# Optimization experiments

Measured on AMD Instinct MI355X. Metric: run time of the kernel, lower is better.

The kernel has to match this reference:

```python
import jax, jax.numpy as jnp
import numpy as np

B, Q, S, D, H, F = 16, 8, 4096, 2048, 16, 128  # batch, new tokens, past kv, d_state, heads, head_dim
W_SCALE = 0.02  # keep projections well-conditioned for stable softmax


def setup_inputs() -> dict:
    key = jax.random.key(0)
    ks = jax.random.split(key, 8)
    return {
        "x": jax.random.normal(ks[0], (B, Q, D), jnp.float32),
        "cache_k": jax.random.normal(ks[1], (B, S, H, F), jnp.float32),
        "cache_v": jax.random.normal(ks[2], (B, S, H, F), jnp.float32),
        "wq": jax.random.normal(ks[3], (D, H, F), jnp.float32) * W_SCALE,
        "bq": jnp.zeros((H, F), jnp.float32),
        "wk": jax.random.normal(ks[4], (D, H, F), jnp.float32) * W_SCALE,
        "bk": jnp.zeros((H, F), jnp.float32),
        "wv": jax.random.normal(ks[5], (D, H, F), jnp.float32) * W_SCALE,
        "bv": jnp.zeros((H, F), jnp.float32),
        "wo": jax.random.normal(ks[6], (H, F, D), jnp.float32) * W_SCALE,
        "bo": jnp.zeros((D,), jnp.float32),
    }


def reference(x, cache_k, cache_v, wq, bq, wk, bk, wv, bv, wo, bo):
    # QKV projections: DenseGeneral(features=(H, F), axis=-1)
    q = jnp.einsum("bqd,dhf->bqhf", x, wq) + bq          # [B,Q,H,F]
    k_new = jnp.einsum("bqd,dhf->bqhf", x, wk) + bk      # [B,Q,H,F]
    v_new = jnp.einsum("bqd,dhf->bqhf", x, wv) + bv
    # concat-based KV cache growth along the sequence axis (axis=1)
    k = jnp.concatenate([cache_k, k_new], axis=1)        # [B,S+Q,H,F]
    v = jnp.concatenate([cache_v, v_new], axis=1)
    # full dot-product attention over the whole cache (mask=None on decode path)
    scale = 1.0 / jnp.sqrt(jnp.asarray(F, q.dtype))
    scores = jnp.einsum("bqhf,bkhf->bhqk", q, k) * scale  # [B,H,Q,S+Q]
    probs = jax.nn.softmax(scores, axis=-1)
    attn = jnp.einsum("bhqk,bkhf->bhqf", probs, v)        # [B,H,Q,F]
    # output projection: DenseGeneral(features=D, axis=(-3,-1)) contracts (H, F)
    out = jnp.einsum("bhqf,hfd->bqd", attn, wo) + bo      # [B,Q,D]
    return (out, k, v)
```

## Files before the change

kernel.cpp:

```cpp
#include <hip/hip_runtime.h>
#include <hip/hip_bf16.h>

constexpr int Bc = 16;
constexpr int Qc = 8;
constexpr int Sc = 4096;
constexpr int Dc = 2048;
constexpr int Hc = 16;
constexpr int Fc = 128;
constexpr int SP = Sc + Qc;
constexpr int Mr = Bc * Qc;
constexpr int CHUNK = 512;
constexpr int NCHUNK = 9;
constexpr float SCALE = 0.08838834764831845f;
constexpr float LOG2E = 1.4426950408889634f;
constexpr float QSCALE = SCALE * LOG2E;
constexpr int GKS = 8;
constexpr int GKC = Dc / GKS;

typedef float floatx4 __attribute__((ext_vector_type(4)));

__device__ __forceinline__ float4 nt_load4(const float* p) {
    floatx4 r = __builtin_nontemporal_load(reinterpret_cast<const floatx4*>(p));
    return make_float4(r.x, r.y, r.z, r.w);
}
__device__ __forceinline__ void nt_store4(float* p, float4 v) {
    floatx4 r; r.x = v.x; r.y = v.y; r.z = v.z; r.w = v.w;
    __builtin_nontemporal_store(r, reinterpret_cast<floatx4*>(p));
}

__global__ __launch_bounds__(256)
void gemm_ksplit(const float* __restrict__ A, const float* __restrict__ W0,
                 const float* __restrict__ W1, const float* __restrict__ W2,
                 float* __restrict__ part)
{
    const int ntile = blockIdx.x;
    const int mat   = blockIdx.y;
    const int kz    = blockIdx.z;
    const float* __restrict__ W = (mat == 0) ? W0 : ((mat == 1) ? W1 : W2);
    const int t  = threadIdx.x;
    const int tx = t & 15, ty = t >> 4;
    const int r0 = ty * 8, c0 = tx * 8;
    const int ncol0 = ntile * 128;

    __shared__ float a_s[128][17];
    __shared__ float w_s[16][128];

    float acc[8][8] = {};

    const int kbase = kz * GKC;
    for (int k0 = kbase; k0 < kbase + GKC; k0 += 16) {
        {
            const int kk = t & 15, r = t >> 4;
            #pragma unroll
            for (int i = 0; i < 8; i++)
                a_s[r + i * 16][kk] = A[(size_t)(r + i * 16) * Dc + k0 + kk];
        }
        {
            const int nn = t & 127, ks_ = t >> 7;
            #pragma unroll
            for (int i = 0; i < 8; i++)
                w_s[ks_ + i * 2][nn] = W[(size_t)(k0 + ks_ + i * 2) * 2048 + ncol0 + nn];
        }
        __syncthreads();
        #pragma unroll
        for (int kk = 0; kk < 16; kk++) {
            float av[8], wv[8];
            #pragma unroll
            for (int i = 0; i < 8; i++) av[i] = a_s[r0 + i][kk];
            #pragma unroll
            for (int j = 0; j < 8; j++) wv[j] = w_s[kk][c0 + j];
            #pragma unroll
            for (int i = 0; i < 8; i++)
                #pragma unroll
                for (int j = 0; j < 8; j++)
                    acc[i][j] += av[i] * wv[j];
        }
        __syncthreads();
    }
    float* __restrict__ dst = part + (size_t)(mat * GKS + kz) * Mr * 2048;
    #pragma unroll
    for (int i = 0; i < 8; i++)
        #pragma unroll
        for (int j = 0; j < 8; j++)
            dst[(size_t)(r0 + i) * 2048 + ncol0 + c0 + j] = acc[i][j];
}

__global__ __launch_bounds__(256)
void reduce_qkv(const float* __restrict__ part, const float* __restrict__ bq,
                const float* __restrict__ bk, const float* __restrict__ bv,
                float* __restrict__ q_ws, float* __restrict__ out_k, float* __restrict__ out_v)
{
    const int mat = blockIdx.y;
    const int e4 = blockIdx.x * 256 + threadIdx.x;
    const int e = e4 * 4;
    const int m = e >> 11, n = e & 2047;
    const float* __restrict__ p = part + (size_t)mat * GKS * (Mr * 2048);
    float4 s = make_float4(0, 0, 0, 0);
    #pragma unroll
    for (int ks = 0; ks < GKS; ks++) {
        const float4 a = *reinterpret_cast<const float4*>(&p[(size_t)ks * (Mr * 2048) + e]);
        s.x += a.x; s.y += a.y; s.z += a.z; s.w += a.w;
    }
    const int b = m >> 3, qi = m & 7;
    if (mat == 0) {
        const float4 bb = *reinterpret_cast<const float4*>(&bq[n]);
        s.x += bb.x; s.y += bb.y; s.z += bb.z; s.w += bb.w;
        *reinterpret_cast<float4*>(&q_ws[e]) = s;
    } else if (mat == 1) {
        const float4 bb = *reinterpret_cast<const float4*>(&bk[n]);
        s.x += bb.x; s.y += bb.y; s.z += bb.z; s.w += bb.w;
        *reinterpret_cast<float4*>(&out_k[((size_t)(b * SP + Sc + qi)) * 2048 + n]) = s;
    } else {
        const float4 bb = *reinterpret_cast<const float4*>(&bv[n]);
        s.x += bb.x; s.y += bb.y; s.z += bb.z; s.w += bb.w;
        *reinterpret_cast<float4*>(&out_v[((size_t)(b * SP + Sc + qi)) * 2048 + n]) = s;
    }
}

template<bool TAIL, int LEN>
__global__ __launch_bounds__(256, 3)
void attn_fused(const float* __restrict__ cache_k, const float* __restrict__ cache_v,
                const float* __restrict__ q_ws,
                float* __restrict__ out_k, float* __restrict__ out_v,
                float* __restrict__ part_acc, float* __restrict__ part_l)
{
    const int c = TAIL ? 8 : blockIdx.x;
    const int h = blockIdx.y;
    const int b = blockIdx.z;
    const int t = threadIdx.x;
    const int w = t >> 6;
    const int lane = t & 63;
    const int half = lane >> 5;
    const int fl = lane & 31;
    const int s0 = c * CHUNK;

    constexpr int kpw = LEN / 4;
    constexpr int pairs = LEN / 8;

    __shared__ float wacc[4][Qc][Fc];
    __shared__ float l_w[4][Qc];

    const int sel1 = fl & 1, sel2 = (fl >> 1) & 1, sel3 = (fl >> 2) & 1;
    const int myqi = 4 * sel1 + 2 * sel2 + sel3;
    int baddr[Qc];
    #pragma unroll
    for (int qi = 0; qi < Qc; qi++) {
        const int slot = ((qi >> 2) & 1) | (((qi >> 1) & 1) << 1) | ((qi & 1) << 2);
        baddr[qi] = (lane & ~7) | slot;
    }

    float4 qreg[Qc];
    #pragma unroll
    for (int qi = 0; qi < Qc; qi++) {
        float4 qv = *reinterpret_cast<const float4*>(
            &q_ws[((size_t)(b * Qc + qi)) * Dc + h * Fc + fl * 4]);
        qv.x *= QSCALE; qv.y *= QSCALE; qv.z *= QSCALE; qv.w *= QSCALE;
        qreg[qi] = qv;
    }

    float4 acc[Qc];
    float lsum = 0.f;
    #pragma unroll
    for (int i = 0; i < Qc; i++) acc[i] = make_float4(0, 0, 0, 0);

    #pragma unroll 4
    for (int j = 0; j < pairs; j++) {
        const int kl = w * kpw + 2 * j + half;
        const int key = s0 + kl;
        const size_t outoff = (((size_t)b * SP + key) * Hc + h) * Fc + fl * 4;
        float4 kv, vv;
        if (!TAIL) {
            const size_t coff = (((size_t)b * Sc + key) * Hc + h) * Fc + fl * 4;
            kv = nt_load4(&cache_k[coff]);
            vv = nt_load4(&cache_v[coff]);
            nt_store4(&out_k[outoff], kv);
            nt_store4(&out_v[outoff], vv);
        } else {
            kv = *reinterpret_cast<const float4*>(&out_k[outoff]);
            vv = *reinterpret_cast<const float4*>(&out_v[outoff]);
        }
        float p[Qc];
        #pragma unroll
        for (int qi = 0; qi < Qc; qi++)
            p[qi] = kv.x * qreg[qi].x + kv.y * qreg[qi].y
                  + kv.z * qreg[qi].z + kv.w * qreg[qi].w;
        float a1[4];
        #pragma unroll
        for (int i = 0; i < 4; i++) {
            const float send = sel1 ? p[i] : p[i + 4];
            const float keep = sel1 ? p[i + 4] : p[i];
            a1[i] = keep + __shfl_xor(send, 1, 64);
        }
        float a2[2];
        #pragma unroll
        for (int i = 0; i < 2; i++) {
            const float send = sel2 ? a1[i] : a1[i + 2];
            const float keep = sel2 ? a1[i + 2] : a1[i];
            a2[i] = keep + __shfl_xor(send, 2, 64);
        }
        float s_ = (sel3 ? a2[1] : a2[0]) + __shfl_xor(sel3 ? a2[0] : a2[1], 4, 64);
        s_ += __shfl_xor(s_, 8, 64);
        s_ += __shfl_xor(s_, 16, 64);
        const float e = __builtin_amdgcn_exp2f(s_);
        lsum += e;
        #pragma unroll
        for (int qi = 0; qi < Qc; qi++) {
            const float pe = __shfl(e, baddr[qi], 64);
            acc[qi].x += pe * vv.x; acc[qi].y += pe * vv.y;
            acc[qi].z += pe * vv.z; acc[qi].w += pe * vv.w;
        }
    }

    #pragma unroll
    for (int qi = 0; qi < Qc; qi++) {
        acc[qi].x += __shfl_xor(acc[qi].x, 32, 64);
        acc[qi].y += __shfl_xor(acc[qi].y, 32, 64);
        acc[qi].z += __shfl_xor(acc[qi].z, 32, 64);
        acc[qi].w += __shfl_xor(acc[qi].w, 32, 64);
    }
    lsum += __shfl_xor(lsum, 32, 64);
    if (half == 0) {
        #pragma unroll
        for (int qi = 0; qi < Qc; qi++)
            *reinterpret_cast<float4*>(&wacc[w][qi][fl * 4]) = acc[qi];
    }
    if (lane < 8) l_w[w][4 * (lane & 1) + 2 * ((lane >> 1) & 1) + ((lane >> 2) & 1)] = lsum;
    __syncthreads();

    {
        const int qi = t >> 5, f4 = (t & 31) * 4;
        float4 s_ = make_float4(0, 0, 0, 0);
        #pragma unroll
        for (int ww = 0; ww < 4; ww++) {
            const float4 a = *reinterpret_cast<const float4*>(&wacc[ww][qi][f4]);
            s_.x += a.x; s_.y += a.y; s_.z += a.z; s_.w += a.w;
        }
        const size_t idx = (size_t)(b * Hc + h) * NCHUNK + c;
        *reinterpret_cast<float4*>(&part_acc[(idx * Qc + qi) * Fc + f4]) = s_;
        if ((t & 31) == 0)
            part_l[idx * Qc + qi] = l_w[0][qi] + l_w[1][qi] + l_w[2][qi] + l_w[3][qi];
    }
}

__global__ __launch_bounds__(256)
void attn_combine(const float* __restrict__ part_acc, const float* __restrict__ part_l,
                  float* __restrict__ attn_ws)
{
    const int bh = blockIdx.x;
    const int b = bh >> 4, h = bh & 15;
    const int t = threadIdx.x;
    const int qi = t >> 5, f4 = (t & 31) * 4;
    const size_t base = (size_t)bh * NCHUNK;

    float lg = 0.f;
    #pragma unroll
    for (int c = 0; c < NCHUNK; c++) lg += part_l[(base + c) * Qc + qi];
    float4 s_ = make_float4(0, 0, 0, 0);
    #pragma unroll
    for (int c = 0; c < NCHUNK; c++) {
        const float4 a = *reinterpret_cast<const float4*>(
            &part_acc[((base + c) * Qc + qi) * Fc + f4]);
        s_.x += a.x; s_.y += a.y; s_.z += a.z; s_.w += a.w;
    }
    const float inv = 1.0f / lg;
    const float4 o = make_float4(s_.x * inv, s_.y * inv, s_.z * inv, s_.w * inv);
    *reinterpret_cast<float4*>(&attn_ws[((size_t)(b * Qc + qi)) * Dc + h * Fc + f4]) = o;
}

__global__ __launch_bounds__(256)
void reduce_o(const float* __restrict__ part, const float* __restrict__ bo,
              float* __restrict__ out)
{
    const int e4 = blockIdx.x * 256 + threadIdx.x;
    const int e = e4 * 4;
    const int n = e & 2047;
    float4 s = make_float4(0, 0, 0, 0);
    #pragma unroll
    for (int ks = 0; ks < GKS; ks++) {
        const float4 a = *reinterpret_cast<const float4*>(&part[(size_t)ks * (Mr * 2048) + e]);
        s.x += a.x; s.y += a.y; s.z += a.z; s.w += a.w;
    }
    const float4 bb = *reinterpret_cast<const float4*>(&bo[n]);
    s.x += bb.x; s.y += bb.y; s.z += bb.z; s.w += bb.w;
    *reinterpret_cast<float4*>(&out[e]) = s;
}

extern "C" void kernel_launch(void* const* d_in, const int* in_sizes, int n_in,
                              void* d_out, int out_size, void* d_ws, size_t ws_size,
                              hipStream_t stream)
{
    (void)in_sizes; (void)n_in; (void)out_size; (void)ws_size;
    const float* x       = (const float*)d_in[0];
    const float* cache_k = (const float*)d_in[1];
    const float* cache_v = (const float*)d_in[2];
    const float* wq      = (const float*)d_in[3];
    const float* bq      = (const float*)d_in[4];
    const float* wk      = (const float*)d_in[5];
    const float* bk      = (const float*)d_in[6];
    const float* wv      = (const float*)d_in[7];
    const float* bv      = (const float*)d_in[8];
    const float* wo      = (const float*)d_in[9];
    const float* bo      = (const float*)d_in[10];

    float* out   = (float*)d_out;
    float* out_k = out + (size_t)Mr * Dc;
    float* out_v = out_k + (size_t)Bc * SP * Hc * Fc;

    float* ws       = (float*)d_ws;
    float* q_ws     = ws;
    float* attn_ws  = ws + 262144;
    float* part_l   = ws + 524288;
    float* gemm_part = ws + 557056;
    float* part_acc = gemm_part;

    gemm_ksplit<<<dim3(16, 3, GKS), 256, 0, stream>>>(x, wq, wk, wv, gemm_part);
    reduce_qkv<<<dim3(256, 3), 256, 0, stream>>>(gemm_part, bq, bk, bv, q_ws, out_k, out_v);
    attn_fused<false, CHUNK><<<dim3(8, Hc, Bc), 256, 0, stream>>>(
        cache_k, cache_v, q_ws, out_k, out_v, part_acc, part_l);
    attn_fused<true, 8><<<dim3(1, Hc, Bc), 256, 0, stream>>>(
        cache_k, cache_v, q_ws, out_k, out_v, part_acc, part_l);
    attn_combine<<<dim3(Bc * Hc), 256, 0, stream>>>(part_acc, part_l, attn_ws);
    gemm_ksplit<<<dim3(16, 1, GKS), 256, 0, stream>>>(attn_ws, wo, wo, wo, gemm_part);
    reduce_o<<<dim3(256), 256, 0, stream>>>(gemm_part, bo, out);
}
```

Before: 533.1 us.

## Process all heads per block with contiguous key rows and fold tail chunk

```diff
diff --git a/kernel.cpp b/kernel.cpp
--- a/kernel.cpp
+++ b/kernel.cpp
@@ -9,8 +9,8 @@
 constexpr int Fc = 128;
 constexpr int SP = Sc + Qc;
 constexpr int Mr = Bc * Qc;
-constexpr int CHUNK = 512;
-constexpr int NCHUNK = 9;
+constexpr int CHUNK = 256;
+constexpr int NCHUNK = 16;
 constexpr float SCALE = 0.08838834764831845f;
 constexpr float LOG2E = 1.4426950408889634f;
 constexpr float QSCALE = SCALE * LOG2E;
@@ -117,28 +117,24 @@
     }
 }
 
-template<bool TAIL, int LEN>
-__global__ __launch_bounds__(256, 3)
+__global__ __launch_bounds__(1024, 4)
 void attn_fused(const float* __restrict__ cache_k, const float* __restrict__ cache_v,
                 const float* __restrict__ q_ws,
                 float* __restrict__ out_k, float* __restrict__ out_v,
                 float* __restrict__ part_acc, float* __restrict__ part_l)
 {
-    const int c = TAIL ? 8 : blockIdx.x;
-    const int h = blockIdx.y;
-    const int b = blockIdx.z;
+    const int c = blockIdx.x;
+    const int b = blockIdx.y;
     const int t = threadIdx.x;
-    const int w = t >> 6;
     const int lane = t & 63;
-    const int half = lane >> 5;
+    const int hwid = t >> 5;
+    const int h = hwid & 15;
+    const int par = hwid >> 4;
     const int fl = lane & 31;
     const int s0 = c * CHUNK;
 
-    constexpr int kpw = LEN / 4;
-    constexpr int pairs = LEN / 8;
-
-    __shared__ float wacc[4][Qc][Fc];
-    __shared__ float l_w[4][Qc];
+    __shared__ float wacc_s[Hc][Qc][Fc];
+    __shared__ float l_s[Hc][Qc];
 
     const int sel1 = fl & 1, sel2 = (fl >> 1) & 1, sel3 = (fl >> 2) & 1;
     const int myqi = 4 * sel1 + 2 * sel2 + sel3;
@@ -163,22 +159,18 @@
     #pragma unroll
     for (int i = 0; i < Qc; i++) acc[i] = make_float4(0, 0, 0, 0);
 
-    #pragma unroll 4
-    for (int j = 0; j < pairs; j++) {
-        const int kl = w * kpw + 2 * j + half;
-        const int key = s0 + kl;
-        const size_t outoff = (((size_t)b * SP + key) * Hc + h) * Fc + fl * 4;
-        float4 kv, vv;
-        if (!TAIL) {
-            const size_t coff = (((size_t)b * Sc + key) * Hc + h) * Fc + fl * 4;
-            kv = nt_load4(&cache_k[coff]);
-            vv = nt_load4(&cache_v[coff]);
-            nt_store4(&out_k[outoff], kv);
-            nt_store4(&out_v[outoff], vv);
-        } else {
-            kv = *reinterpret_cast<const float4*>(&out_k[outoff]);
-            vv = *reinterpret_cast<const float4*>(&out_v[outoff]);
-        }
+    const int rowoff = h * Fc + fl * 4;
+
+    #pragma unroll 2
+    for (int n = 0; n < CHUNK / 2; n++) {
+        const int key = s0 + 2 * n + par;
+        const size_t coff = ((size_t)(b * Sc + key)) * 2048 + rowoff;
+        const size_t ooff = ((size_t)(b * SP + key)) * 2048 + rowoff;
+        const float4 kv = nt_load4(&cache_k[coff]);
+        const float4 vv = nt_load4(&cache_v[coff]);
+        nt_store4(&out_k[ooff], kv);
+        nt_store4(&out_v[ooff], vv);
+
         float p[Qc];
         #pragma unroll
         for (int qi = 0; qi < Qc; qi++)
@@ -211,34 +203,65 @@
         }
     }
 
-    #pragma unroll
-    for (int qi = 0; qi < Qc; qi++) {
-        acc[qi].x += __shfl_xor(acc[qi].x, 32, 64);
-        acc[qi].y += __shfl_xor(acc[qi].y, 32, 64);
-        acc[qi].z += __shfl_xor(acc[qi].z, 32, 64);
-        acc[qi].w += __shfl_xor(acc[qi].w, 32, 64);
-    }
-    lsum += __shfl_xor(lsum, 32, 64);
-    if (half == 0) {
+    if (c == NCHUNK - 1) {
+        #pragma unroll
+        for (int m = 0; m < Qc / 2; m++) {
+            const int key = Sc + 2 * m + par;
+            const size_t ooff = ((size_t)(b * SP + key)) * 2048 + rowoff;
+            const float4 kv = *reinterpret_cast<const float4*>(&out_k[ooff]);
+            const float4 vv = *reinterpret_cast<const float4*>(&out_v[ooff]);
+
+            float p[Qc];
+            #pragma unroll
+            for (int qi = 0; qi < Qc; qi++)
+                p[qi] = kv.x * qreg[qi].x + kv.y * qreg[qi].y
+                      + kv.z * qreg[qi].z + kv.w * qreg[qi].w;
+            float a1[4];
+            #pragma unroll
+            for (int i = 0; i < 4; i++) {
+                const float send = sel1 ? p[i] : p[i + 4];
+                const float keep = sel1 ? p[i + 4] : p[i];
+                a1[i] = keep + __shfl_xor(send, 1, 64);
+            }
+            float a2[2];
+            #pragma unroll
+            for (int i = 0; i < 2; i++) {
+                const float send = sel2 ? a1[i] : a1[i + 2];
+                const float keep = sel2 ? a1[i + 2] : a1[i];
+                a2[i] = keep + __shfl_xor(send, 2, 64);
+            }
+            float s_ = (sel3 ? a2[1] : a2[0]) + __shfl_xor(sel3 ? a2[0] : a2[1], 4, 64);
+            s_ += __shfl_xor(s_, 8, 64);
+            s_ += __shfl_xor(s_, 16, 64);
+            const float e = __builtin_amdgcn_exp2f(s_);
+            lsum += e;
+            #pragma unroll
+            for (int qi = 0; qi < Qc; qi++) {
+                const float pe = __shfl(e, baddr[qi], 64);
+                acc[qi].x += pe * vv.x; acc[qi].y += pe * vv.y;
+                acc[qi].z += pe * vv.z; acc[qi].w += pe * vv.w;
+            }
+        }
+    }
+
+    if (par == 0) {
         #pragma unroll
         for (int qi = 0; qi < Qc; qi++)
-            *reinterpret_cast<float4*>(&wacc[w][qi][fl * 4]) = acc[qi];
-    }
-    if (lane < 8) l_w[w][4 * (lane & 1) + 2 * ((lane >> 1) & 1) + ((lane >> 2) & 1)] = lsum;
+            *reinterpret_cast<float4*>(&wacc_s[h][qi][fl * 4]) = acc[qi];
+        if (fl < 8) l_s[h][myqi] = lsum;
+    }
     __syncthreads();
-
-    {
-        const int qi = t >> 5, f4 = (t & 31) * 4;
-        float4 s_ = make_float4(0, 0, 0, 0);
-        #pragma unroll
-        for (int ww = 0; ww < 4; ww++) {
-            const float4 a = *reinterpret_cast<const float4*>(&wacc[ww][qi][f4]);
-            s_.x += a.x; s_.y += a.y; s_.z += a.z; s_.w += a.w;
-        }
+    if (par == 1) {
         const size_t idx = (size_t)(b * Hc + h) * NCHUNK + c;
-        *reinterpret_cast<float4*>(&part_acc[(idx * Qc + qi) * Fc + f4]) = s_;
-        if ((t & 31) == 0)
-            part_l[idx * Qc + qi] = l_w[0][qi] + l_w[1][qi] + l_w[2][qi] + l_w[3][qi];
+        #pragma unroll
+        for (int qi = 0; qi < Qc; qi++) {
+            const float4 a = *reinterpret_cast<const float4*>(&wacc_s[h][qi][fl * 4]);
+            float4 s_;
+            s_.x = a.x + acc[qi].x; s_.y = a.y + acc[qi].y;
+            s_.z = a.z + acc[qi].z; s_.w = a.w + acc[qi].w;
+            *reinterpret_cast<float4*>(&part_acc[(idx * Qc + qi) * Fc + fl * 4]) = s_;
+        }
+        if (fl < 8) part_l[idx * Qc + myqi] = l_s[h][myqi] + lsum;
     }
 }
 
@@ -315,9 +338,7 @@
 
     gemm_ksplit<<<dim3(16, 3, GKS), 256, 0, stream>>>(x, wq, wk, wv, gemm_part);
     reduce_qkv<<<dim3(256, 3), 256, 0, stream>>>(gemm_part, bq, bk, bv, q_ws, out_k, out_v);
-    attn_fused<false, CHUNK><<<dim3(8, Hc, Bc), 256, 0, stream>>>(
-        cache_k, cache_v, q_ws, out_k, out_v, part_acc, part_l);
-    attn_fused<true, 8><<<dim3(1, Hc, Bc), 256, 0, stream>>>(
+    attn_fused<<<dim3(NCHUNK, Bc), 1024, 0, stream>>>(
         cache_k, cache_v, q_ws, out_k, out_v, part_acc, part_l);
     attn_combine<<<dim3(Bc * Hc), 256, 0, stream>>>(part_acc, part_l, attn_ws);
     gemm_ksplit<<<dim3(16, 1, GKS), 256, 0, stream>>>(attn_ws, wo, wo, wo, gemm_part);
```

New measurement: 516.9 us. 1.03x faster.
